# Optimization experiments

Hardware: AMD Instinct MI355X
Metric: run time of the kernel (lower is better)

## Reference

```python
import jax, jax.numpy as jnp
import numpy as np

B, N, DQ, DK, DV = 8, 2048, 1024, 1024, 1024

def setup_inputs() -> dict:
    key = jax.random.key(0)
    kx, kq, kk, kv = jax.random.split(key, 4)
    x = jax.random.normal(kx, (B, N, DQ), dtype=jnp.float32)
    # nn.Linear(dim_q, dim_k, bias=False) weights: [out, in]
    s = 1.0 / np.sqrt(DQ)
    Wq = jax.random.uniform(kq, (DK, DQ), jnp.float32, -s, s)
    Wk = jax.random.uniform(kk, (DK, DQ), jnp.float32, -s, s)
    Wv = jax.random.uniform(kv, (DV, DQ), jnp.float32, -s, s)
    return {"x": x, "Wq": Wq, "Wk": Wk, "Wv": Wv}

def reference(x, Wq, Wk, Wv):
    batch, n, _ = x.shape
    q = jnp.einsum('bnd,kd->bnk', x, Wq)  # [B,n,DK]
    k = jnp.einsum('bnd,kd->bnk', x, Wk)  # [B,n,DK]
    v = jnp.einsum('bnd,vd->bnv', x, Wv)  # [B,n,DV]
    norm = 1.0 / jnp.sqrt(jnp.asarray(Wq.shape[0], jnp.float32))
    dist = jnp.einsum('bik,bjk->bij', q, k) * norm  # [B,n,n]
    causal = jnp.tril(jnp.ones((n, n), dtype=bool))
    dist = jnp.where(causal[None, :, :], dist, jnp.float32(-1e20))
    dist = jax.nn.softmax(dist, axis=-1)
    att = jnp.einsum('bij,bjv->biv', dist, v)  # [B,n,DV]
    return att
```

## Files before the change

kernel.cpp:

```cpp
#include <hip/hip_runtime.h>
#include <hip/hip_bf16.h>

typedef __attribute__((ext_vector_type(4))) float floatx4;
typedef __bf16 bf16x8 __attribute__((ext_vector_type(8)));
typedef unsigned int u32;
typedef unsigned short u16;

typedef __attribute__((address_space(1))) const u32 g_u32;
typedef __attribute__((address_space(3))) u32 l_u32;

__device__ __forceinline__ u16 f32_to_bf16(float f) {
    union { float f; u32 u; } x{f};
    u32 u = x.u;
    u32 r = (u + 0x7fffu + ((u >> 16) & 1u)) >> 16;
    return (u16)r;
}


__device__ __forceinline__ void stage_half_sw(const u16* gbase, int ld, u16* lds_half, int tid) {
    int lane = tid & 63;
    int rsub = lane >> 3;
    int colsw = ((lane & 7) ^ rsub) << 3;
#pragma unroll
    for (int j = 0; j < 2; ++j) {
        int q = (tid >> 6) * 2 + j;
        int row = q * 8 + rsub;
        const u16* g = gbase + (long)row * ld + colsw;
        u16* l = lds_half + q * 512 + lane * 8;
        __builtin_amdgcn_global_load_lds((g_u32*)g, (l_u32*)l, 16, 0, 0);
    }
}

#define EIGHT_PHASE_K1024_LOOP(Ab, Bb, lda, ldb)                                       \
    stage_half_sw(Bb,                  ldb, &Bs[0][0],        tid);                    \
    stage_half_sw(Bb + 128 * (ldb),    ldb, &Bs[0][128 * 64], tid);                    \
    stage_half_sw(Ab,                  lda, &As[0][0],        tid);                    \
    stage_half_sw(Ab + 128 * (lda),    lda, &As[0][128 * 64], tid);                    \
    stage_half_sw(Bb + 64,             ldb, &Bs[1][0],        tid);                    \
    stage_half_sw(Bb + 64 + 128 * (ldb), ldb, &Bs[1][128 * 64], tid);                  \
    asm volatile("s_waitcnt vmcnt(4)" ::: "memory");                                   \
    __builtin_amdgcn_sched_barrier(0);                                                 \
    __builtin_amdgcn_s_barrier();                                                      \
    for (int i = 0; i < 8; ++i) {                                                      \
        int t1  = 2 * i + 1;                                                           \
        int tn  = (2 * i + 2 <= 15) ? 2 * i + 2 : 15;                                  \
        int tn1 = (2 * i + 3 <= 15) ? 2 * i + 3 : 15;                                  \
        const u16* gA1 = Ab + t1 * 64;                                                 \
        const u16* gB2 = Bb + tn * 64;                                                 \
        const u16* gA2 = Ab + tn * 64;                                                 \
        const u16* gB3 = Bb + tn1 * 64;                                                \
        bf16x8 bq0[4], bq1[4];                                                         \
        _Pragma("unroll")                                                              \
        for (int half = 0; half < 2; ++half) {                                         \
            _Pragma("unroll")                                                          \
            for (int p = 0; p < 4; ++p) {                                              \
                if (p == 0) {                                                          \
                    _Pragma("unroll")                                                  \
                    for (int ni = 0; ni < 4; ++ni) {                                   \
                        bq0[ni] = *(const bf16x8*)&Bs[half][brow + ni * 1024 + sl0];   \
                        bq1[ni] = *(const bf16x8*)&Bs[half][brow + ni * 1024 + sl1];   \
                    }                                                                  \
                }                                                                      \
                bf16x8 a00 = *(const bf16x8*)&As[half][arow + (2 * p)     * 1024 + sl0]; \
                bf16x8 a01 = *(const bf16x8*)&As[half][arow + (2 * p)     * 1024 + sl1]; \
                bf16x8 a10 = *(const bf16x8*)&As[half][arow + (2 * p + 1) * 1024 + sl0]; \
                bf16x8 a11 = *(const bf16x8*)&As[half][arow + (2 * p + 1) * 1024 + sl1]; \
                int ph = half * 4 + p;                                                 \
                switch (ph) {                                                          \
                    case 0: stage_half_sw(gA1,              lda, &As[1][0],        tid); break; \
                    case 1: stage_half_sw(gA1 + 128 * (lda), lda, &As[1][128 * 64], tid); break; \
                    case 2: stage_half_sw(gB2,              ldb, &Bs[0][0],        tid); break; \
                    case 3: stage_half_sw(gB2 + 128 * (ldb), ldb, &Bs[0][128 * 64], tid); break; \
                    case 4: stage_half_sw(gA2,              lda, &As[0][0],        tid); break; \
                    case 5: stage_half_sw(gA2 + 128 * (lda), lda, &As[0][128 * 64], tid); break; \
                    case 6: stage_half_sw(gB3,              ldb, &Bs[1][0],        tid); break; \
                    case 7: stage_half_sw(gB3 + 128 * (ldb), ldb, &Bs[1][128 * 64], tid); break; \
                }                                                                      \
                __builtin_amdgcn_s_barrier();                                          \
                __builtin_amdgcn_s_setprio(1);                                         \
                int m0 = 2 * p;                                                        \
                _Pragma("unroll")                                                      \
                for (int ni = 0; ni < 4; ++ni) {                                       \
                    acc[m0][ni]     = __builtin_amdgcn_mfma_f32_16x16x32_bf16(a00, bq0[ni], acc[m0][ni],     0, 0, 0); \
                    acc[m0][ni]     = __builtin_amdgcn_mfma_f32_16x16x32_bf16(a01, bq1[ni], acc[m0][ni],     0, 0, 0); \
                    acc[m0 + 1][ni] = __builtin_amdgcn_mfma_f32_16x16x32_bf16(a10, bq0[ni], acc[m0 + 1][ni], 0, 0, 0); \
                    acc[m0 + 1][ni] = __builtin_amdgcn_mfma_f32_16x16x32_bf16(a11, bq1[ni], acc[m0 + 1][ni], 0, 0, 0); \
                }                                                                      \
                __builtin_amdgcn_s_setprio(0);                                         \
                if (p == 3) {                                                          \
                    asm volatile("s_waitcnt vmcnt(4)" ::: "memory");                   \
                    __builtin_amdgcn_sched_barrier(0);                                 \
                }                                                                      \
                __builtin_amdgcn_s_barrier();                                          \
            }                                                                          \
        }                                                                              \
    }                                                                                  \
    asm volatile("s_waitcnt vmcnt(0)" ::: "memory");                                   \
    __builtin_amdgcn_sched_barrier(0);

__global__ __launch_bounds__(512, 2)
void qkv_gemm8(const u16* __restrict__ A, const u16* __restrict__ Bw,
               u16* __restrict__ QKi, u16* __restrict__ Vt)
{
    __shared__ u16 As[2][256 * 64];
    __shared__ u16 Bs[2][256 * 64];

    int bid = blockIdx.x;
    int wg = (bid & 7) * 96 + (bid >> 3);
    int mt = wg / 12, nt = wg - mt * 12;

    int tid = threadIdx.x;
    int lane = tid & 63, wv = tid >> 6;
    int wr = wv >> 2, wc = wv & 3;
    int lrow = lane & 15, quad = lane >> 4;
    int sw = lrow & 7;

    const u16* Ab = A + (long)mt * 256 * 1024;
    const u16* Bb = Bw + (long)nt * 256 * 1024;

    floatx4 acc[8][4] = {};
    const int arow = (wr * 128 + lrow) * 64;
    const int brow = (wc * 64 + lrow) * 64;
    const int sl0 = (quad ^ sw) * 8;
    const int sl1 = ((4 + quad) ^ sw) * 8;

    EIGHT_PHASE_K1024_LOOP(Ab, Bb, 1024, 1024)

    if (nt < 8) {
        long crow0 = (long)mt * 256 + wr * 128 + quad * 4;
        int  ccol0 = nt * 256 + wc * 64 + lrow;
#pragma unroll
        for (int mi = 0; mi < 8; ++mi) {
#pragma unroll
            for (int r = 0; r < 4; ++r) {
                long row = crow0 + mi * 16 + r;
#pragma unroll
                for (int ni = 0; ni < 4; ++ni)
                    QKi[row * 2048 + ccol0 + ni * 16] = f32_to_bf16(acc[mi][ni][r]);
            }
        }
    } else {
        int dv0   = (nt - 8) * 256 + wc * 64 + lrow;
        long tok0 = (long)mt * 256 + wr * 128 + quad * 4;
#pragma unroll
        for (int mi = 0; mi < 8; ++mi) {
#pragma unroll
            for (int ni = 0; ni < 4; ++ni) {
                ushort4 o;
                o.x = f32_to_bf16(acc[mi][ni][0]);
                o.y = f32_to_bf16(acc[mi][ni][1]);
                o.z = f32_to_bf16(acc[mi][ni][2]);
                o.w = f32_to_bf16(acc[mi][ni][3]);
                *(ushort4*)(Vt + (long)(dv0 + ni * 16) * 16384 + tok0 + mi * 16) = o;
            }
        }
    }
}

__global__ __launch_bounds__(512, 2)
void s_gemm8(const u16* __restrict__ QKi, u16* __restrict__ P, float* __restrict__ lsum)
{
    __shared__ u16 As[2][256 * 64];
    __shared__ u16 Bs[2][256 * 64];

    int bid = blockIdx.x;
    int b  = bid & 7;
    int ti = bid >> 3;
    int mt = (int)((__builtin_sqrtf(8.0f * ti + 1.0f) - 1.0f) * 0.5f);
    while ((mt + 1) * (mt + 2) / 2 <= ti) ++mt;
    while (mt * (mt + 1) / 2 > ti) --mt;
    int nt = ti - mt * (mt + 1) / 2;

    int tid = threadIdx.x;
    int lane = tid & 63, wv = tid >> 6;
    int wr = wv >> 2, wc = wv & 3;
    int lrow = lane & 15, quad = lane >> 4;
    int sw = lrow & 7;

    const u16* Qb = QKi + (long)b * 2048 * 2048 + (long)mt * 256 * 2048;
    const u16* Kb = QKi + (long)b * 2048 * 2048 + (long)nt * 256 * 2048 + 1024;
    u16* Pb = P + (long)b * 2048 * 2048;
    float* ls = lsum + b * 2048;

    floatx4 acc[8][4] = {};
    const int arow = (wr * 128 + lrow) * 64;
    const int brow = (wc * 64 + lrow) * 64;
    const int sl0 = (quad ^ sw) * 8;
    const int sl1 = ((4 + quad) ^ sw) * 8;

    EIGHT_PHASE_K1024_LOOP(Qb, Kb, 2048, 2048)

    int crow0 = mt * 256 + wr * 128 + quad * 4;
    int ccol0 = nt * 256 + wc * 64 + lrow;
#pragma unroll
    for (int mi = 0; mi < 8; ++mi) {
#pragma unroll
        for (int r = 0; r < 4; ++r) {
            int row = crow0 + mi * 16 + r;
            float rs = 0.f;
#pragma unroll
            for (int ni = 0; ni < 4; ++ni) {
                int col = ccol0 + ni * 16;
                float v = acc[mi][ni][r] * 0.03125f;
                float e = (col > row) ? 0.f : __expf(v);
                Pb[(long)row * 2048 + col] = f32_to_bf16(e);
                rs += e;
            }
            rs += __shfl_xor(rs, 1, 16);
            rs += __shfl_xor(rs, 2, 16);
            rs += __shfl_xor(rs, 4, 16);
            rs += __shfl_xor(rs, 8, 16);
            if (lrow == 0) atomicAdd(&ls[row], rs);
        }
    }
}

__global__ __launch_bounds__(512)
void pv_gemm2(const u16* __restrict__ P, const u16* __restrict__ Vt,
              float* __restrict__ O, const float* __restrict__ lsum)
{
    __shared__ u16 As[128 * 32];
    __shared__ u16 Bs[256 * 32];
    int b = blockIdx.x, nt = blockIdx.y, mt = 15 - blockIdx.z;
    const u16* Ab = P  + (long)b * 2048 * 2048 + (long)mt * 128 * 2048;
    const u16* Bb = Vt + (long)b * 2048 + (long)nt * 256 * 16384;
    float* Ob = O + (long)b * 2048 * 1024;
    const float* ls = lsum + b * 2048;
    int nkt = mt * 4 + 4;

    int tid = threadIdx.x, lane = tid & 63, wave = tid >> 6;
    int wr = wave >> 2, wc = wave & 3;
    int lrow = lane & 15, quad = lane >> 4;

    {
        int flat = tid * 8, row = flat >> 5, col = flat & 31;
        __builtin_amdgcn_global_load_lds((g_u32*)(Ab + (long)row * 2048 + col),
                                         (l_u32*)&As[flat], 16, 0, 0);
#pragma unroll
        for (int it = 0; it < 2; ++it) {
            int f2 = it * 4096 + tid * 8, r2 = f2 >> 5, c2 = f2 & 31;
            __builtin_amdgcn_global_load_lds((g_u32*)(Bb + (long)r2 * 16384 + c2),
                                             (l_u32*)&Bs[f2], 16, 0, 0);
        }
    }

    floatx4 acc[4][4] = {};
    const int aoff = (wr * 64 + lrow) * 32 + quad * 8;
    const int boff = (wc * 64 + lrow) * 32 + quad * 8;

    for (int kt = 0; kt < nkt; ++kt) {
        __syncthreads();
        bf16x8 af[4], bfr[4];
#pragma unroll
        for (int i = 0; i < 4; ++i) {
            af[i]  = *(const bf16x8*)&As[aoff + i * 16 * 32];
            bfr[i] = *(const bf16x8*)&Bs[boff + i * 16 * 32];
        }
#pragma unroll
        for (int mi = 0; mi < 4; ++mi)
#pragma unroll
            for (int ni = 0; ni < 4; ++ni)
                acc[mi][ni] = __builtin_amdgcn_mfma_f32_16x16x32_bf16(af[mi], bfr[ni], acc[mi][ni], 0, 0, 0);
        __syncthreads();
        if (kt + 1 < nkt) {
            const u16* An = Ab + (kt + 1) * 32;
            const u16* Bn = Bb + (kt + 1) * 32;
            int flat = tid * 8, row = flat >> 5, col = flat & 31;
            __builtin_amdgcn_global_load_lds((g_u32*)(An + (long)row * 2048 + col),
                                             (l_u32*)&As[flat], 16, 0, 0);
#pragma unroll
            for (int it = 0; it < 2; ++it) {
                int f2 = it * 4096 + tid * 8, r2 = f2 >> 5, c2 = f2 & 31;
                __builtin_amdgcn_global_load_lds((g_u32*)(Bn + (long)r2 * 16384 + c2),
                                                 (l_u32*)&Bs[f2], 16, 0, 0);
            }
        }
    }

    int crow0 = mt * 128 + wr * 64 + quad * 4;
    int ccol0 = nt * 256 + wc * 64 + lrow;
#pragma unroll
    for (int mi = 0; mi < 4; ++mi) {
#pragma unroll
        for (int r = 0; r < 4; ++r) {
            int row = crow0 + mi * 16 + r;
            float linv = 1.0f / ls[row];
#pragma unroll
            for (int ni = 0; ni < 4; ++ni)
                Ob[(long)row * 1024 + ccol0 + ni * 16] = acc[mi][ni][r] * linv;
        }
    }
}

__global__ __launch_bounds__(256)
void cvt_f32_bf16(const float* __restrict__ src, u16* __restrict__ dst, long n)
{
    long idx = ((long)blockIdx.x * 256 + threadIdx.x) << 2;
    if (idx >= n) return;
    float4 f = *(const float4*)(src + idx);
    ushort4 o;
    o.x = f32_to_bf16(f.x); o.y = f32_to_bf16(f.y);
    o.z = f32_to_bf16(f.z); o.w = f32_to_bf16(f.w);
    *(ushort4*)(dst + idx) = o;
}

__global__ __launch_bounds__(256)
void cvt_w3(const float* __restrict__ Wq, const float* __restrict__ Wk,
            const float* __restrict__ Wv, u16* __restrict__ dst)
{
    int which = blockIdx.x >> 10;
    const float* src = which == 0 ? Wq : (which == 1 ? Wk : Wv);
    long base = (long)(blockIdx.x & 1023) * 1024 + threadIdx.x * 4;
    float4 f = *(const float4*)(src + base);
    ushort4 o;
    o.x = f32_to_bf16(f.x); o.y = f32_to_bf16(f.y);
    o.z = f32_to_bf16(f.z); o.w = f32_to_bf16(f.w);
    *(ushort4*)(dst + (long)which * 1048576 + base) = o;
}

extern "C" void kernel_launch(void* const* d_in, const int* in_sizes, int n_in,
                              void* d_out, int out_size, void* d_ws, size_t ws_size,
                              hipStream_t stream)
{
    const int B = 8, N = 2048, D = 1024;
    const long MT = (long)B * N;
    const long nX = MT * D;
    const long nW = (long)D * D;

    const float* x  = (const float*)d_in[0];
    const float* Wq = (const float*)d_in[1];
    const float* Wk = (const float*)d_in[2];
    const float* Wv = (const float*)d_in[3];
    float* out = (float*)d_out;

    u16* wb   = (u16*)d_ws;
    u16* xb   = wb + 3 * nW;
    u16* QKi  = xb + nX;
    u16* Vt   = QKi + MT * 2048;
    u16* P    = Vt + nX;
    float* lsum = (float*)wb;

    cvt_f32_bf16<<<(int)(nX / 1024), 256, 0, stream>>>(x, xb, nX);
    cvt_w3<<<3072, 256, 0, stream>>>(Wq, Wk, Wv, wb);

    qkv_gemm8<<<dim3(768, 1, 1), 512, 0, stream>>>(xb, wb, QKi, Vt);

    hipMemsetAsync(lsum, 0, (size_t)B * N * sizeof(float), stream);

    s_gemm8<<<dim3(288, 1, 1), 512, 0, stream>>>(QKi, P, lsum);

    pv_gemm2<<<dim3(8, 4, 16), 512, 0, stream>>>(P, Vt, out, lsum);
}
```

Before: 362.2 us.

## Rewrite PV GEMM with 256x256 eight-phase pipelined tiles and fuse conversion launches

Replaces the simple single-buffered 128x256 PV GEMM with a 256x256-tile kernel that reuses the swizzled double-buffered eight-phase loop from the other GEMMs, parameterized by a causal-dependent iteration count. This aims to raise data reuse and overlap loads with MFMA in the largest-remaining stage. It also merges the x/weight conversion kernels and the lsum memset into one launch, moving lsum to a separate workspace region to cut launch overhead. The trade-off is fewer blocks (256) with uneven causal work, which may hurt load balance.

```diff
diff --git a/kernel.cpp b/kernel.cpp
--- a/kernel.cpp
+++ b/kernel.cpp
@@ -31,7 +31,7 @@
     }
 }
 
-#define EIGHT_PHASE_K1024_LOOP(Ab, Bb, lda, ldb)                                       \
+#define EIGHT_PHASE_LOOP(Ab, Bb, lda, ldb, ITERS, TMAX)                                \
     stage_half_sw(Bb,                  ldb, &Bs[0][0],        tid);                    \
     stage_half_sw(Bb + 128 * (ldb),    ldb, &Bs[0][128 * 64], tid);                    \
     stage_half_sw(Ab,                  lda, &As[0][0],        tid);                    \
@@ -41,10 +41,10 @@
     asm volatile("s_waitcnt vmcnt(4)" ::: "memory");                                   \
     __builtin_amdgcn_sched_barrier(0);                                                 \
     __builtin_amdgcn_s_barrier();                                                      \
-    for (int i = 0; i < 8; ++i) {                                                      \
+    for (int i = 0; i < (ITERS); ++i) {                                                \
         int t1  = 2 * i + 1;                                                           \
-        int tn  = (2 * i + 2 <= 15) ? 2 * i + 2 : 15;                                  \
-        int tn1 = (2 * i + 3 <= 15) ? 2 * i + 3 : 15;                                  \
+        int tn  = (2 * i + 2 <= (TMAX)) ? 2 * i + 2 : (TMAX);                          \
+        int tn1 = (2 * i + 3 <= (TMAX)) ? 2 * i + 3 : (TMAX);                          \
         const u16* gA1 = Ab + t1 * 64;                                                 \
         const u16* gB2 = Bb + tn * 64;                                                 \
         const u16* gA2 = Ab + tn * 64;                                                 \
@@ -124,7 +124,7 @@
     const int sl0 = (quad ^ sw) * 8;
     const int sl1 = ((4 + quad) ^ sw) * 8;
 
-    EIGHT_PHASE_K1024_LOOP(Ab, Bb, 1024, 1024)
+    EIGHT_PHASE_LOOP(Ab, Bb, 1024, 1024, 8, 15)
 
     if (nt < 8) {
         long crow0 = (long)mt * 256 + wr * 128 + quad * 4;
@@ -188,7 +188,7 @@
     const int sl0 = (quad ^ sw) * 8;
     const int sl1 = ((4 + quad) ^ sw) * 8;
 
-    EIGHT_PHASE_K1024_LOOP(Qb, Kb, 2048, 2048)
+    EIGHT_PHASE_LOOP(Qb, Kb, 2048, 2048, 8, 15)
 
     int crow0 = mt * 256 + wr * 128 + quad * 4;
     int ccol0 = nt * 256 + wc * 64 + lrow;
@@ -215,72 +215,45 @@
     }
 }
 
-__global__ __launch_bounds__(512)
-void pv_gemm2(const u16* __restrict__ P, const u16* __restrict__ Vt,
+__global__ __launch_bounds__(512, 2)
+void pv_gemm8(const u16* __restrict__ P, const u16* __restrict__ Vt,
               float* __restrict__ O, const float* __restrict__ lsum)
 {
-    __shared__ u16 As[128 * 32];
-    __shared__ u16 Bs[256 * 32];
-    int b = blockIdx.x, nt = blockIdx.y, mt = 15 - blockIdx.z;
-    const u16* Ab = P  + (long)b * 2048 * 2048 + (long)mt * 128 * 2048;
-    const u16* Bb = Vt + (long)b * 2048 + (long)nt * 256 * 16384;
+    __shared__ u16 As[2][256 * 64];
+    __shared__ u16 Bs[2][256 * 64];
+
+    int bid = blockIdx.x;
+    int b  = bid & 7;
+    int r2 = bid >> 3;
+    int mt = r2 >> 2;
+    int nt = r2 & 3;
+
+    int tid = threadIdx.x;
+    int lane = tid & 63, wv = tid >> 6;
+    int wr = wv >> 2, wc = wv & 3;
+    int lrow = lane & 15, quad = lane >> 4;
+    int sw = lrow & 7;
+
+    const u16* Ab = P  + (long)b * 2048 * 2048 + (long)mt * 256 * 2048;
+    const u16* Bb = Vt + (long)nt * 256 * 16384 + b * 2048;
     float* Ob = O + (long)b * 2048 * 1024;
     const float* ls = lsum + b * 2048;
-    int nkt = mt * 4 + 4;
-
-    int tid = threadIdx.x, lane = tid & 63, wave = tid >> 6;
-    int wr = wave >> 2, wc = wave & 3;
-    int lrow = lane & 15, quad = lane >> 4;
-
-    {
-        int flat = tid * 8, row = flat >> 5, col = flat & 31;
-        __builtin_amdgcn_global_load_lds((g_u32*)(Ab + (long)row * 2048 + col),
-                                         (l_u32*)&As[flat], 16, 0, 0);
-#pragma unroll
-        for (int it = 0; it < 2; ++it) {
-            int f2 = it * 4096 + tid * 8, r2 = f2 >> 5, c2 = f2 & 31;
-            __builtin_amdgcn_global_load_lds((g_u32*)(Bb + (long)r2 * 16384 + c2),
-                                             (l_u32*)&Bs[f2], 16, 0, 0);
-        }
-    }
-
-    floatx4 acc[4][4] = {};
-    const int aoff = (wr * 64 + lrow) * 32 + quad * 8;
-    const int boff = (wc * 64 + lrow) * 32 + quad * 8;
-
-    for (int kt = 0; kt < nkt; ++kt) {
-        __syncthreads();
-        bf16x8 af[4], bfr[4];
-#pragma unroll
-        for (int i = 0; i < 4; ++i) {
-            af[i]  = *(const bf16x8*)&As[aoff + i * 16 * 32];
-            bfr[i] = *(const bf16x8*)&Bs[boff + i * 16 * 32];
-        }
-#pragma unroll
-        for (int mi = 0; mi < 4; ++mi)
-#pragma unroll
-            for (int ni = 0; ni < 4; ++ni)
-                acc[mi][ni] = __builtin_amdgcn_mfma_f32_16x16x32_bf16(af[mi], bfr[ni], acc[mi][ni], 0, 0, 0);
-        __syncthreads();
-        if (kt + 1 < nkt) {
-            const u16* An = Ab + (kt + 1) * 32;
-            const u16* Bn = Bb + (kt + 1) * 32;
-            int flat = tid * 8, row = flat >> 5, col = flat & 31;
-            __builtin_amdgcn_global_load_lds((g_u32*)(An + (long)row * 2048 + col),
-                                             (l_u32*)&As[flat], 16, 0, 0);
-#pragma unroll
-            for (int it = 0; it < 2; ++it) {
-                int f2 = it * 4096 + tid * 8, r2 = f2 >> 5, c2 = f2 & 31;
-                __builtin_amdgcn_global_load_lds((g_u32*)(Bn + (long)r2 * 16384 + c2),
-                                                 (l_u32*)&Bs[f2], 16, 0, 0);
-            }
-        }
-    }
-
-    int crow0 = mt * 128 + wr * 64 + quad * 4;
+
+    int iters = (mt + 1) * 2;
+    int tmax  = (mt + 1) * 4 - 1;
+
+    floatx4 acc[8][4] = {};
+    const int arow = (wr * 128 + lrow) * 64;
+    const int brow = (wc * 64 + lrow) * 64;
+    const int sl0 = (quad ^ sw) * 8;
+    const int sl1 = ((4 + quad) ^ sw) * 8;
+
+    EIGHT_PHASE_LOOP(Ab, Bb, 2048, 16384, iters, tmax)
+
+    int crow0 = mt * 256 + wr * 128 + quad * 4;
     int ccol0 = nt * 256 + wc * 64 + lrow;
 #pragma unroll
-    for (int mi = 0; mi < 4; ++mi) {
+    for (int mi = 0; mi < 8; ++mi) {
 #pragma unroll
         for (int r = 0; r < 4; ++r) {
             int row = crow0 + mi * 16 + r;
@@ -293,29 +266,32 @@
 }
 
 __global__ __launch_bounds__(256)
-void cvt_f32_bf16(const float* __restrict__ src, u16* __restrict__ dst, long n)
-{
-    long idx = ((long)blockIdx.x * 256 + threadIdx.x) << 2;
-    if (idx >= n) return;
-    float4 f = *(const float4*)(src + idx);
-    ushort4 o;
-    o.x = f32_to_bf16(f.x); o.y = f32_to_bf16(f.y);
-    o.z = f32_to_bf16(f.z); o.w = f32_to_bf16(f.w);
-    *(ushort4*)(dst + idx) = o;
-}
-
-__global__ __launch_bounds__(256)
-void cvt_w3(const float* __restrict__ Wq, const float* __restrict__ Wk,
-            const float* __restrict__ Wv, u16* __restrict__ dst)
-{
-    int which = blockIdx.x >> 10;
-    const float* src = which == 0 ? Wq : (which == 1 ? Wk : Wv);
-    long base = (long)(blockIdx.x & 1023) * 1024 + threadIdx.x * 4;
-    float4 f = *(const float4*)(src + base);
-    ushort4 o;
-    o.x = f32_to_bf16(f.x); o.y = f32_to_bf16(f.y);
-    o.z = f32_to_bf16(f.z); o.w = f32_to_bf16(f.w);
-    *(ushort4*)(dst + (long)which * 1048576 + base) = o;
+void cvt_all(const float* __restrict__ x, const float* __restrict__ Wq,
+             const float* __restrict__ Wk, const float* __restrict__ Wv,
+             u16* __restrict__ xb, u16* __restrict__ wb, float* __restrict__ lsum)
+{
+    int bb = blockIdx.x;
+    if (bb < 16384) {
+        long idx = ((long)bb * 256 + threadIdx.x) << 2;
+        float4 f = *(const float4*)(x + idx);
+        ushort4 o;
+        o.x = f32_to_bf16(f.x); o.y = f32_to_bf16(f.y);
+        o.z = f32_to_bf16(f.z); o.w = f32_to_bf16(f.w);
+        *(ushort4*)(xb + idx) = o;
+    } else if (bb < 16384 + 3072) {
+        int wbk = bb - 16384;
+        int which = wbk >> 10;
+        const float* src = which == 0 ? Wq : (which == 1 ? Wk : Wv);
+        long base = (long)(wbk & 1023) * 1024 + threadIdx.x * 4;
+        float4 f = *(const float4*)(src + base);
+        ushort4 o;
+        o.x = f32_to_bf16(f.x); o.y = f32_to_bf16(f.y);
+        o.z = f32_to_bf16(f.z); o.w = f32_to_bf16(f.w);
+        *(ushort4*)(wb + (long)which * 1048576 + base) = o;
+    } else {
+        long idx = ((long)(bb - 16384 - 3072) * 256 + threadIdx.x) << 2;
+        *(float4*)(lsum + idx) = float4{0.f, 0.f, 0.f, 0.f};
+    }
 }
 
 extern "C" void kernel_launch(void* const* d_in, const int* in_sizes, int n_in,
@@ -338,16 +314,13 @@
     u16* QKi  = xb + nX;
     u16* Vt   = QKi + MT * 2048;
     u16* P    = Vt + nX;
-    float* lsum = (float*)wb;
-
-    cvt_f32_bf16<<<(int)(nX / 1024), 256, 0, stream>>>(x, xb, nX);
-    cvt_w3<<<3072, 256, 0, stream>>>(Wq, Wk, Wv, wb);
+    float* lsum = (float*)(P + (long)B * N * N);
+
+    cvt_all<<<16384 + 3072 + 16, 256, 0, stream>>>(x, Wq, Wk, Wv, xb, wb, lsum);
 
     qkv_gemm8<<<dim3(768, 1, 1), 512, 0, stream>>>(xb, wb, QKi, Vt);
 
-    hipMemsetAsync(lsum, 0, (size_t)B * N * sizeof(float), stream);
-
     s_gemm8<<<dim3(288, 1, 1), 512, 0, stream>>>(QKi, P, lsum);
 
-    pv_gemm2<<<dim3(8, 4, 16), 512, 0, stream>>>(P, Vt, out, lsum);
-}
+    pv_gemm8<<<dim3(256, 1, 1), 512, 0, stream>>>(P, Vt, out, lsum);
+}
```

Result: faster. 350.0 us (-3.4%).
